# Performance work log

Measured on AMD Instinct MI355X. Metric: run time of the kernel, lower is better.

The kernel has to match this reference:

```python
import jax, jax.numpy as jnp
import numpy as np


def setup_inputs() -> dict:
    B, S, DK, DV, H = 2, 2048, 1024, 1024, 16
    ks = jax.random.split(jax.random.key(0), 7)
    keys = jax.random.normal(ks[0], (B, S, DK), jnp.float32)
    queries = jax.random.normal(ks[1], (B, S, DK), jnp.float32)
    values = jax.random.normal(ks[2], (B, S, DV), jnp.float32)
    # per-head projection weights, stored as [H, in, out] (torch Linear uses W.T; math-equivalent)
    WQ = jax.random.normal(ks[3], (H, DK, DK // H), jnp.float32) / np.sqrt(DK).astype(np.float32)
    WK = jax.random.normal(ks[4], (H, DK, DK // H), jnp.float32) / np.sqrt(DK).astype(np.float32)
    WV = jax.random.normal(ks[5], (H, DV, DV // H), jnp.float32) / np.sqrt(DV).astype(np.float32)
    WO = jax.random.normal(ks[6], (DV, DV), jnp.float32) / np.sqrt(DV).astype(np.float32)
    return {"keys": keys, "queries": queries, "values": values,
            "WQ": WQ, "WK": WK, "WV": WV, "WO": WO, "masking": 1}


def reference(keys, queries, values, WQ, WK, WV, WO, masking):
    B, Sq, _ = queries.shape
    Sk = keys.shape[1]
    # batched per-head projections (original loops over heads in Python)
    Q = jnp.einsum('bqd,hde->bhqe', queries, WQ)   # [B,H,Sq,dh]
    K = jnp.einsum('bkd,hde->bhke', keys, WK)      # [B,H,Sk,dh]
    V = jnp.einsum('bkd,hde->bhke', values, WV)    # [B,H,Sk,dvh]
    q_idx = jnp.arange(Sq)[:, None]
    k_idx = jnp.arange(Sk)[None, :]
    causal = k_idx <= q_idx
    # NOTE: original never applies the slope m; bias = (i - j) for i<=j else 0, same for all heads
    bias = jnp.where(causal, (k_idx - q_idx).astype(jnp.float32), 0.0)
    scale = np.float32(1.0 / np.sqrt(Sk))  # original divides by sqrt(keys.shape[1])
    y = (jnp.einsum('bhqe,bhke->bhqk', Q, K) + bias) * scale
    if masking:
        y = jnp.where(causal, y, -jnp.inf)
    # original: F.softmax(y, 1) on [B,Sq,Sk] -> softmax over the QUERY axis
    z = jax.nn.softmax(y, axis=2)
    out = jnp.einsum('bhqk,bhke->bhqe', z, V)      # [B,H,Sq,dvh]
    out = out.transpose(0, 2, 1, 3).reshape(B, Sq, -1)  # concat heads on last dim
    return out @ WO
```

## Files before the change

### kernel.cpp

```cpp
#include <hip/hip_runtime.h>
#include <math.h>

#define SEQ    2048
#define DMODEL 1024
#define NH     16
#define DH     64
#define NB     2
#define BHN    (NB*NH)

static constexpr float SCALE = 0.02209708691207961f;

typedef __attribute__((ext_vector_type(8))) short short8;
typedef __attribute__((ext_vector_type(4))) short short4v;
typedef __attribute__((ext_vector_type(4))) float f32x4;

__device__ __forceinline__ short f2bf(float f) {
    union { float f; unsigned u; } v; v.f = f;
    unsigned r = (v.u + 0x7FFFu + ((v.u >> 16) & 1u)) >> 16;
    return (short)r;
}

__device__ __forceinline__ unsigned pack_bf2(float a, float b) {
    union { float f; unsigned u; } ua, ub; ua.f = a; ub.f = b;
    return __builtin_amdgcn_perm(ub.u + 0x8000u, ua.u + 0x8000u, 0x07060302u);
}

__device__ __forceinline__ float bf2f(short s) {
    union { unsigned u; float f; } v; v.u = ((unsigned)(unsigned short)s) << 16;
    return v.f;
}

__device__ __forceinline__ void load16_lds(const short* g, short* l) {
    __builtin_amdgcn_global_load_lds(
        (const __attribute__((address_space(1))) unsigned int*)g,
        (__attribute__((address_space(3))) unsigned int*)l,
        16, 0, 0);
}

__device__ __forceinline__ void stage_rows(const short* g, short* s, int t, int ldg, int nIter) {
    int wave = t >> 6, lane = t & 63;
    #pragma unroll
    for (int i = 0; i < 4; ++i) {
        if (i >= nIter) break;
        int E   = i * 2048 + wave * 512 + lane * 8;
        int row = E >> 6;
        int blk = (lane & 7) ^ (row & 7);
        load16_lds(g + (size_t)row * ldg + blk * 8, s + i * 2048 + wave * 512);
    }
}

__device__ __forceinline__ short8 frag_sw(const short* s, int rowbase, int ks, int lane) {
    int m   = rowbase + (lane & 15);
    int q   = lane >> 4;
    int blk = (ks * 4 + q) ^ (m & 7);
    return *(const short8*)(s + m * 64 + blk * 8);
}

__device__ __forceinline__ void swizzle_tile(int x, int y, int& tile, int& bh) {
    int r = y >> 3;
    bh = (y & 7) * 4 + r;
    int xs = (r & 2) ? ((x + 16) & 31) : x;
    tile = (r & 1) ? (31 - xs) : xs;
}

__global__ __launch_bounds__(256) void convert_x(
    const float* __restrict__ q, const float* __restrict__ k, const float* __restrict__ v,
    short* __restrict__ Xq, short* __restrict__ Xk, short* __restrict__ Xv)
{
    const int z = blockIdx.z;
    const float* src = (z == 0) ? q : (z == 1) ? k : v;
    short* dst = (z == 0) ? Xq : (z == 1) ? Xk : Xv;
    size_t idx = ((size_t)blockIdx.x * 256 + threadIdx.x) * 8;
    float4 a = *(const float4*)(src + idx);
    float4 b = *(const float4*)(src + idx + 4);
    short8 o;
    o[0] = f2bf(a.x); o[1] = f2bf(a.y); o[2] = f2bf(a.z); o[3] = f2bf(a.w);
    o[4] = f2bf(b.x); o[5] = f2bf(b.y); o[6] = f2bf(b.z); o[7] = f2bf(b.w);
    *(short8*)(dst + idx) = o;
}

__global__ __launch_bounds__(256) void convert_w(
    const float* __restrict__ WQ, const float* __restrict__ WK,
    const float* __restrict__ WV, const float* __restrict__ WO,
    short* __restrict__ WQt, short* __restrict__ WKt,
    short* __restrict__ WVt, short* __restrict__ WOt)
{
    const int z = blockIdx.z;
    const int k0 = blockIdx.x * 64;
    const int ny = blockIdx.y;
    const float* W = (z == 0) ? WQ : (z == 1) ? WK : (z == 2) ? WV : WO;
    short* Wt = (z == 0) ? WQt : (z == 1) ? WKt : (z == 2) ? WVt : WOt;

    __shared__ float Ts[64][68];
    const int t = threadIdx.x;
    const int tr = t >> 4, tc4 = (t & 15) * 4;

    #pragma unroll
    for (int i = 0; i < 4; ++i) {
        int row = tr + i * 16;
        float4 v;
        if (z < 3) v = *(const float4*)(W + (size_t)ny * DMODEL * DH + (size_t)(k0 + row) * DH + tc4);
        else       v = *(const float4*)(W + (size_t)(k0 + row) * DMODEL + ny * 64 + tc4);
        Ts[tc4 + 0][row] = v.x; Ts[tc4 + 1][row] = v.y;
        Ts[tc4 + 2][row] = v.z; Ts[tc4 + 3][row] = v.w;
    }
    __syncthreads();
    #pragma unroll
    for (int i = 0; i < 4; ++i) {
        int nl = tr + i * 16;
        short4v o;
        o[0] = f2bf(Ts[nl][tc4 + 0]); o[1] = f2bf(Ts[nl][tc4 + 1]);
        o[2] = f2bf(Ts[nl][tc4 + 2]); o[3] = f2bf(Ts[nl][tc4 + 3]);
        *(short4v*)(Wt + (size_t)(ny * 64 + nl) * DMODEL + k0 + tc4) = o;
    }
}

__global__ __launch_bounds__(256) void gemm_nt(
    const short* __restrict__ A0, const short* __restrict__ A1, const short* __restrict__ A2,
    const short* __restrict__ B0, const short* __restrict__ B1, const short* __restrict__ B2,
    short* __restrict__ Y0, short* __restrict__ Y1, short* __restrict__ Y2,
    float* __restrict__ outF, int phase)
{
    const int z = blockIdx.z;
    const short* X  = (phase == 1) ? A0 : (z == 0) ? A0 : (z == 1) ? A1 : A2;
    const short* Wt = (phase == 1) ? B0 : (z == 0) ? B0 : (z == 1) ? B1 : B2;
    short* Y        = (z == 0) ? Y0 : (z == 1) ? Y1 : Y2;
    const bool vOrient = (phase == 0) && (z == 2);

    const int n0 = blockIdx.x * 128;
    const int m0 = blockIdx.y * 128;

    __shared__ short As[128 * 64];
    __shared__ short Bs[128 * 64];

    const int t = threadIdx.x;
    const int wave = t >> 6, lane = t & 63;
    const int wrow = (wave >> 1) * 64, wcol = (wave & 1) * 64;
    const int quad = lane >> 4, l15 = lane & 15;

    f32x4 acc[4][4];
    #pragma unroll
    for (int i = 0; i < 4; ++i)
        #pragma unroll
        for (int j = 0; j < 4; ++j)
            acc[i][j] = (f32x4)0.f;

    for (int k0 = 0; k0 < DMODEL; k0 += 64) {
        __syncthreads();
        stage_rows(X  + (size_t)m0 * DMODEL + k0, As, t, DMODEL, 4);
        stage_rows(Wt + (size_t)n0 * DMODEL + k0, Bs, t, DMODEL, 4);
        __syncthreads();
        if (!vOrient) {
            #pragma unroll
            for (int ks = 0; ks < 2; ++ks) {
                short8 xf[4], wf[4];
                #pragma unroll
                for (int i = 0; i < 4; ++i) xf[i] = frag_sw(As, wrow + i * 16, ks, lane);
                #pragma unroll
                for (int i = 0; i < 4; ++i) wf[i] = frag_sw(Bs, wcol + i * 16, ks, lane);
                #pragma unroll
                for (int a = 0; a < 4; ++a)
                    #pragma unroll
                    for (int b = 0; b < 4; ++b)
                        acc[a][b] = __builtin_amdgcn_mfma_f32_16x16x32_bf16(
                            wf[a], xf[b], acc[a][b], 0, 0, 0);
            }
        } else {
            #pragma unroll
            for (int ks = 0; ks < 2; ++ks) {
                short8 xf[4], wf[4];
                #pragma unroll
                for (int i = 0; i < 4; ++i) xf[i] = frag_sw(As, wrow + i * 16, ks, lane);
                #pragma unroll
                for (int i = 0; i < 4; ++i) wf[i] = frag_sw(Bs, wcol + i * 16, ks, lane);
                #pragma unroll
                for (int a = 0; a < 4; ++a)
                    #pragma unroll
                    for (int b = 0; b < 4; ++b)
                        acc[a][b] = __builtin_amdgcn_mfma_f32_16x16x32_bf16(
                            xf[a], wf[b], acc[a][b], 0, 0, 0);
            }
        }
    }

    if (vOrient) {
        #pragma unroll
        for (int a = 0; a < 4; ++a) {
            #pragma unroll
            for (int b = 0; b < 4; ++b) {
                int m = m0 + wrow + a * 16 + quad * 4;
                int n = n0 + wcol + b * 16 + l15;
                int bb = m >> 11, s = m & 2047, h = n >> 6, e = n & 63;
                short4v o;
                #pragma unroll
                for (int i = 0; i < 4; ++i) o[i] = f2bf(acc[a][b][i]);
                *(short4v*)(Y + ((size_t)((bb * NH + h) * DH + e)) * SEQ + s) = o;
            }
        }
    } else if (phase == 1) {
        #pragma unroll
        for (int a = 0; a < 4; ++a) {
            #pragma unroll
            for (int b = 0; b < 4; ++b) {
                int n = n0 + wcol + a * 16 + quad * 4;
                int m = m0 + wrow + b * 16 + l15;
                float4 o = make_float4(acc[a][b][0], acc[a][b][1], acc[a][b][2], acc[a][b][3]);
                *(float4*)(outF + (size_t)m * DMODEL + n) = o;
            }
        }
    } else {
        #pragma unroll
        for (int a = 0; a < 4; ++a) {
            #pragma unroll
            for (int b = 0; b < 4; ++b) {
                int n = n0 + wcol + a * 16 + quad * 4;
                int m = m0 + wrow + b * 16 + l15;
                int bb = m >> 11, s = m & 2047, h = n >> 6, e = n & 63;
                short4v o;
                #pragma unroll
                for (int i = 0; i < 4; ++i) o[i] = f2bf(acc[a][b][i]);
                *(short4v*)(Y + ((size_t)((bb * NH + h) * SEQ + s)) * DH + e) = o;
            }
        }
    }
}

template<int MODE>
__device__ __forceinline__ void stats_tile_w(
    const short* Qbuf, const short8 Kf[2], const float bias[4][4],
    float dsum[4], int lane, int wave16)
{
    const int quad = lane >> 4, l15 = lane & 15;
    f32x4 acc[4];
    #pragma unroll
    for (int nt = 0; nt < 4; ++nt) acc[nt] = (f32x4)0.f;
    #pragma unroll
    for (int ks = 0; ks < 2; ++ks) {
        #pragma unroll
        for (int nt = 0; nt < 4; ++nt)
            acc[nt] = __builtin_amdgcn_mfma_f32_16x16x32_bf16(
                Kf[ks], frag_sw(Qbuf, nt * 16, ks, lane), acc[nt], 0, 0, 0);
    }
    #pragma unroll
    for (int nt = 0; nt < 4; ++nt) {
        #pragma unroll
        for (int i = 0; i < 4; ++i) {
            float bi = bias[nt][i];
            float v = (MODE == 2) ? fmaf(acc[nt][i], SCALE, fminf(bi, 0.f))
                                  : fmaf(acc[nt][i], SCALE, bi);
            float e = __expf(v);
            if (MODE == 1)
                e = ((wave16 + quad * 4 + i) <= (nt * 16 + l15)) ? e : 0.f;
            dsum[i] += e;
        }
    }
}

__global__ __launch_bounds__(256) void stats_mfma(
    const short* __restrict__ Qg, const short* __restrict__ Kg,
    float* __restrict__ rDg, const int* __restrict__ mask_p)
{
    int kt, bh;
    swizzle_tile(blockIdx.x, blockIdx.y, kt, bh);
    const int k0 = kt * 64;
    const int masking = mask_p[0];

    __shared__ short Ks[64 * 64];
    __shared__ short Qs[2][64 * 64];

    const int t = threadIdx.x;
    const int wave = t >> 6, lane = t & 63;
    const int quad = lane >> 4, l15 = lane & 15;

    const int q0s = masking ? k0 : 0;
    stage_rows(Kg + ((size_t)bh * SEQ + k0) * DH, Ks, t, DH, 2);
    stage_rows(Qg + ((size_t)bh * SEQ + q0s) * DH, Qs[0], t, DH, 2);
    __syncthreads();

    short8 Kf[2];
    Kf[0] = frag_sw(Ks, wave * 16, 0, lane);
    Kf[1] = frag_sw(Ks, wave * 16, 1, lane);

    float bias[4][4];
    #pragma unroll
    for (int nt = 0; nt < 4; ++nt)
        #pragma unroll
        for (int i = 0; i < 4; ++i)
            bias[nt][i] = SCALE * (float)((k0 + wave * 16 + quad * 4 + i)
                                        - (q0s + nt * 16 + l15));

    float dsum[4] = {0.f, 0.f, 0.f, 0.f};
    const int nIter = (SEQ - q0s) / 64;
    for (int it = 0; it < nIter; ++it) {
        const int cur = it & 1;
        if (it > 0) __syncthreads();
        if (it + 1 < nIter)
            stage_rows(Qg + ((size_t)bh * SEQ + q0s + (it + 1) * 64) * DH, Qs[1 - cur], t, DH, 2);
        if (!masking)      stats_tile_w<2>(Qs[cur], Kf, bias, dsum, lane, wave * 16);
        else if (it == 0)  stats_tile_w<1>(Qs[cur], Kf, bias, dsum, lane, wave * 16);
        else               stats_tile_w<0>(Qs[cur], Kf, bias, dsum, lane, wave * 16);
        #pragma unroll
        for (int nt = 0; nt < 4; ++nt)
            #pragma unroll
            for (int i = 0; i < 4; ++i)
                bias[nt][i] -= 64.f * SCALE;
    }

    #pragma unroll
    for (int i = 0; i < 4; ++i) {
        float d = dsum[i];
        #pragma unroll
        for (int mm = 1; mm < 16; mm <<= 1) d += __shfl_xor(d, mm);
        dsum[i] = d;
    }
    if (l15 == 0) {
        const int kc = k0 + wave * 16 + quad * 4;
        float4 o = make_float4(1.f / dsum[0], 1.f / dsum[1], 1.f / dsum[2], 1.f / dsum[3]);
        *(float4*)(rDg + (size_t)bh * SEQ + kc) = o;
    }
}

__global__ __launch_bounds__(256) void scale_vt(
    short* __restrict__ Vt, const float* __restrict__ rDg)
{
    size_t base = ((size_t)blockIdx.x * 256 + threadIdx.x) * 8;
    int s = (int)(base & (SEQ - 1));
    int bh = (int)(base >> 17);
    short8 v = *(short8*)(Vt + base);
    const float* rp = rDg + (size_t)bh * SEQ + s;
    float4 r0 = *(const float4*)rp;
    float4 r1 = *(const float4*)(rp + 4);
    float rr[8] = {r0.x, r0.y, r0.z, r0.w, r1.x, r1.y, r1.z, r1.w};
    union { unsigned u[4]; short8 s8; } o;
    #pragma unroll
    for (int j = 0; j < 4; ++j)
        o.u[j] = pack_bf2(bf2f(v[2 * j]) * rr[2 * j], bf2f(v[2 * j + 1]) * rr[2 * j + 1]);
    *(short8*)(Vt + base) = o.s8;
}

template<int MODE>
__device__ __forceinline__ void attn_tile(
    const short* Kbuf, const short* Vbuf, short* Pw,
    const short8 Qf[2], const float bias[4][4], f32x4 oacc[4],
    int lane, int quad, int l15, int qloc)
{
    f32x4 sacc[4];
    #pragma unroll
    for (int mt = 0; mt < 4; ++mt) sacc[mt] = (f32x4)0.f;
    #pragma unroll
    for (int ks = 0; ks < 2; ++ks) {
        #pragma unroll
        for (int mt = 0; mt < 4; ++mt)
            sacc[mt] = __builtin_amdgcn_mfma_f32_16x16x32_bf16(
                frag_sw(Kbuf, mt * 16, ks, lane), Qf[ks], sacc[mt], 0, 0, 0);
    }
    __asm__ volatile("" ::: "memory");
    #pragma unroll
    for (int mt = 0; mt < 4; ++mt) {
        float p[4];
        #pragma unroll
        for (int i = 0; i < 4; ++i) {
            float bi = bias[mt][i];
            float v = (MODE == 2) ? fmaf(sacc[mt][i], SCALE, fminf(bi, 0.f))
                                  : fmaf(sacc[mt][i], SCALE, bi);
            float e = __expf(v);
            if (MODE == 1)
                e = ((mt * 16 + quad * 4 + i) <= qloc) ? e : 0.f;
            p[i] = e;
        }
        int blk = (2 * mt + (quad >> 1)) ^ (l15 & 7);
        *(uint2*)(Pw + l15 * 64 + blk * 8 + (quad & 1) * 4) =
            make_uint2(pack_bf2(p[0], p[1]), pack_bf2(p[2], p[3]));
    }
    __asm__ volatile("" ::: "memory");
    #pragma unroll
    for (int ks = 0; ks < 2; ++ks) {
        short8 pf = *(const short8*)(Pw + l15 * 64 + (((ks * 4 + quad) ^ (l15 & 7)) * 8));
        #pragma unroll
        for (int mt = 0; mt < 4; ++mt)
            oacc[mt] = __builtin_amdgcn_mfma_f32_16x16x32_bf16(
                frag_sw(Vbuf, mt * 16, ks, lane), pf, oacc[mt], 0, 0, 0);
    }
}

__global__ __launch_bounds__(256) void attn_mfma(
    const short* __restrict__ Qg, const short* __restrict__ Kg, const short* __restrict__ Vt,
    short* __restrict__ attnb, const int* __restrict__ mask_p)
{
    int qt, bh;
    swizzle_tile(blockIdx.x, blockIdx.y, qt, bh);
    const int b = bh / NH, h = bh % NH;
    const int q0 = qt * 64;
    const int masking = mask_p[0];

    __shared__ short Qs[64 * 64];
    __shared__ short Ks[2][64 * 64];
    __shared__ short Vts[2][64 * 64];

    const int t = threadIdx.x;
    const int wave = t >> 6, lane = t & 63;
    const int quad = lane >> 4, l15 = lane & 15;
    short* Pw = Qs + wave * 1024;
    const int qloc = wave * 16 + l15;

    stage_rows(Qg + ((size_t)bh * SEQ + q0) * DH, Qs, t, DH, 2);
    stage_rows(Kg + (size_t)bh * SEQ * DH, Ks[0], t, DH, 2);
    stage_rows(Vt + (size_t)bh * DH * SEQ, Vts[0], t, SEQ, 2);
    __syncthreads();

    short8 Qf[2];
    Qf[0] = frag_sw(Qs, wave * 16, 0, lane);
    Qf[1] = frag_sw(Qs, wave * 16, 1, lane);

    float bias[4][4];
    #pragma unroll
    for (int mt = 0; mt < 4; ++mt)
        #pragma unroll
        for (int i = 0; i < 4; ++i)
            bias[mt][i] = SCALE * (float)((mt * 16 + quad * 4 + i)
                                        - (q0 + qloc));

    f32x4 oacc[4];
    #pragma unroll
    for (int mt = 0; mt < 4; ++mt) oacc[mt] = (f32x4)0.f;

    const int nIter = masking ? (qt + 1) : (SEQ / 64);
    for (int it = 0; it < nIter; ++it) {
        const int cur = it & 1;
        if (it > 0) __syncthreads();
        if (it + 1 < nIter) {
            const int k0n = (it + 1) * 64;
            stage_rows(Kg + ((size_t)bh * SEQ + k0n) * DH, Ks[1 - cur], t, DH, 2);
            stage_rows(Vt + (size_t)bh * DH * SEQ + k0n, Vts[1 - cur], t, SEQ, 2);
        }
        if (!masking)       attn_tile<2>(Ks[cur], Vts[cur], Pw, Qf, bias, oacc, lane, quad, l15, qloc);
        else if (it == qt)  attn_tile<1>(Ks[cur], Vts[cur], Pw, Qf, bias, oacc, lane, quad, l15, qloc);
        else                attn_tile<0>(Ks[cur], Vts[cur], Pw, Qf, bias, oacc, lane, quad, l15, qloc);
        #pragma unroll
        for (int mt = 0; mt < 4; ++mt)
            #pragma unroll
            for (int i = 0; i < 4; ++i)
                bias[mt][i] += 64.f * SCALE;
    }

    #pragma unroll
    for (int mt = 0; mt < 4; ++mt) {
        int e = mt * 16 + quad * 4;
        int q = q0 + wave * 16 + l15;
        short4v o;
        #pragma unroll
        for (int i = 0; i < 4; ++i) o[i] = f2bf(oacc[mt][i]);
        *(short4v*)(attnb + ((size_t)(b * SEQ + q)) * DMODEL + h * DH + e) = o;
    }
}

extern "C" void kernel_launch(void* const* d_in, const int* in_sizes, int n_in,
                              void* d_out, int out_size, void* d_ws, size_t ws_size,
                              hipStream_t stream) {
    const float* keys    = (const float*)d_in[0];
    const float* queries = (const float*)d_in[1];
    const float* values  = (const float*)d_in[2];
    const float* WQ      = (const float*)d_in[3];
    const float* WK      = (const float*)d_in[4];
    const float* WV      = (const float*)d_in[5];
    const float* WO      = (const float*)d_in[6];
    const int*   mask_p  = (const int*)d_in[7];
    float* out = (float*)d_out;

    const size_t nX = (size_t)NB * SEQ * DMODEL;
    const size_t nW = (size_t)DMODEL * DMODEL;
    const size_t nQ = (size_t)BHN * SEQ * DH;

    short* ws = (short*)d_ws;
    short* Xq    = ws;
    short* Xk    = Xq + nX;
    short* Xv    = Xk + nX;
    short* WQt   = Xv + nX;
    short* WKt   = WQt + nW;
    short* WVt   = WKt + nW;
    short* WOt   = WVt + nW;
    short* Qg    = WOt + nW;
    short* Kg    = Qg + nQ;
    short* Vtg   = Kg + nQ;
    short* attnb = Vtg + nQ;
    float* rDg   = (float*)(attnb + nX);

    convert_x<<<dim3(2048, 1, 3), dim3(256), 0, stream>>>(queries, keys, values, Xq, Xk, Xv);
    convert_w<<<dim3(16, 16, 4), dim3(256), 0, stream>>>(WQ, WK, WV, WO, WQt, WKt, WVt, WOt);
    gemm_nt<<<dim3(8, 32, 3), dim3(256), 0, stream>>>(
        Xq, Xk, Xv, WQt, WKt, WVt, Qg, Kg, Vtg, nullptr, 0);
    stats_mfma<<<dim3(32, 32), dim3(256), 0, stream>>>(Qg, Kg, rDg, mask_p);
    scale_vt<<<dim3(2048), dim3(256), 0, stream>>>(Vtg, rDg);
    attn_mfma<<<dim3(32, 32), dim3(256), 0, stream>>>(Qg, Kg, Vtg, attnb, mask_p);
    gemm_nt<<<dim3(8, 32, 1), dim3(256), 0, stream>>>(
        attnb, nullptr, nullptr, WOt, nullptr, nullptr, nullptr, nullptr, nullptr, out, 1);
}
```

Baseline: 268.7 us.

## Fuse V scaling into stats kernel, use exp2, drop attention double buffering

The stats kernel now keeps the per-key reciprocal softmax denominators in shared memory and scales its own 64-column slice of Vt in place. This removes the separate scale_vt launch and the rD global buffer. Both softmax exponentials switch to exp2f, with log2(e) folded into the scale and bias constants. The attention kernel drops K/V double buffering in favour of a single buffer with two barriers per iteration, which cuts LDS use and may raise occupancy but loses overlap of loads with compute.

```diff
diff --git a/kernel.cpp b/kernel.cpp
--- a/kernel.cpp
+++ b/kernel.cpp
@@ -8,7 +8,8 @@
 #define NB     2
 #define BHN    (NB*NH)
 
-static constexpr float SCALE = 0.02209708691207961f;
+static constexpr float SCALE  = 0.02209708691207961f;
+static constexpr float SCALE2 = 0.02209708691207961f * 1.4426950408889634f;
 
 typedef __attribute__((ext_vector_type(8))) short short8;
 typedef __attribute__((ext_vector_type(4))) short short4v;
@@ -246,9 +247,9 @@
         #pragma unroll
         for (int i = 0; i < 4; ++i) {
             float bi = bias[nt][i];
-            float v = (MODE == 2) ? fmaf(acc[nt][i], SCALE, fminf(bi, 0.f))
-                                  : fmaf(acc[nt][i], SCALE, bi);
-            float e = __expf(v);
+            float v = (MODE == 2) ? fmaf(acc[nt][i], SCALE2, fminf(bi, 0.f))
+                                  : fmaf(acc[nt][i], SCALE2, bi);
+            float e = exp2f(v);
             if (MODE == 1)
                 e = ((wave16 + quad * 4 + i) <= (nt * 16 + l15)) ? e : 0.f;
             dsum[i] += e;
@@ -258,7 +259,7 @@
 
 __global__ __launch_bounds__(256) void stats_mfma(
     const short* __restrict__ Qg, const short* __restrict__ Kg,
-    float* __restrict__ rDg, const int* __restrict__ mask_p)
+    short* __restrict__ Vt, const int* __restrict__ mask_p)
 {
     int kt, bh;
     swizzle_tile(blockIdx.x, blockIdx.y, kt, bh);
@@ -267,6 +268,7 @@
 
     __shared__ short Ks[64 * 64];
     __shared__ short Qs[2][64 * 64];
+    __shared__ float rDs[64];
 
     const int t = threadIdx.x;
     const int wave = t >> 6, lane = t & 63;
@@ -286,8 +288,8 @@
     for (int nt = 0; nt < 4; ++nt)
         #pragma unroll
         for (int i = 0; i < 4; ++i)
-            bias[nt][i] = SCALE * (float)((k0 + wave * 16 + quad * 4 + i)
-                                        - (q0s + nt * 16 + l15));
+            bias[nt][i] = SCALE2 * (float)((k0 + wave * 16 + quad * 4 + i)
+                                         - (q0s + nt * 16 + l15));
 
     float dsum[4] = {0.f, 0.f, 0.f, 0.f};
     const int nIter = (SEQ - q0s) / 64;
@@ -303,7 +305,7 @@
         for (int nt = 0; nt < 4; ++nt)
             #pragma unroll
             for (int i = 0; i < 4; ++i)
-                bias[nt][i] -= 64.f * SCALE;
+                bias[nt][i] -= 64.f * SCALE2;
     }
 
     #pragma unroll
@@ -314,28 +316,25 @@
         dsum[i] = d;
     }
     if (l15 == 0) {
-        const int kc = k0 + wave * 16 + quad * 4;
+        const int kloc = wave * 16 + quad * 4;
         float4 o = make_float4(1.f / dsum[0], 1.f / dsum[1], 1.f / dsum[2], 1.f / dsum[3]);
-        *(float4*)(rDg + (size_t)bh * SEQ + kc) = o;
-    }
-}
-
-__global__ __launch_bounds__(256) void scale_vt(
-    short* __restrict__ Vt, const float* __restrict__ rDg)
-{
-    size_t base = ((size_t)blockIdx.x * 256 + threadIdx.x) * 8;
-    int s = (int)(base & (SEQ - 1));
-    int bh = (int)(base >> 17);
-    short8 v = *(short8*)(Vt + base);
-    const float* rp = rDg + (size_t)bh * SEQ + s;
-    float4 r0 = *(const float4*)rp;
-    float4 r1 = *(const float4*)(rp + 4);
-    float rr[8] = {r0.x, r0.y, r0.z, r0.w, r1.x, r1.y, r1.z, r1.w};
-    union { unsigned u[4]; short8 s8; } o;
-    #pragma unroll
-    for (int j = 0; j < 4; ++j)
-        o.u[j] = pack_bf2(bf2f(v[2 * j]) * rr[2 * j], bf2f(v[2 * j + 1]) * rr[2 * j + 1]);
-    *(short8*)(Vt + base) = o.s8;
+        *(float4*)&rDs[kloc] = o;
+    }
+    __syncthreads();
+
+    short* vp = Vt + (size_t)bh * DH * SEQ + k0;
+    #pragma unroll
+    for (int c = t; c < 512; c += 256) {
+        int e = c >> 3, sc = (c & 7) * 8;
+        short* p = vp + (size_t)e * SEQ + sc;
+        short8 v = *(short8*)p;
+        union { unsigned u[4]; short8 s8; } o;
+        #pragma unroll
+        for (int j = 0; j < 4; ++j)
+            o.u[j] = pack_bf2(bf2f(v[2 * j]) * rDs[sc + 2 * j],
+                              bf2f(v[2 * j + 1]) * rDs[sc + 2 * j + 1]);
+        *(short8*)p = o.s8;
+    }
 }
 
 template<int MODE>
@@ -361,9 +360,9 @@
         #pragma unroll
         for (int i = 0; i < 4; ++i) {
             float bi = bias[mt][i];
-            float v = (MODE == 2) ? fmaf(sacc[mt][i], SCALE, fminf(bi, 0.f))
-                                  : fmaf(sacc[mt][i], SCALE, bi);
-            float e = __expf(v);
+            float v = (MODE == 2) ? fmaf(sacc[mt][i], SCALE2, fminf(bi, 0.f))
+                                  : fmaf(sacc[mt][i], SCALE2, bi);
+            float e = exp2f(v);
             if (MODE == 1)
                 e = ((mt * 16 + quad * 4 + i) <= qloc) ? e : 0.f;
             p[i] = e;
@@ -394,8 +393,8 @@
     const int masking = mask_p[0];
 
     __shared__ short Qs[64 * 64];
-    __shared__ short Ks[2][64 * 64];
-    __shared__ short Vts[2][64 * 64];
+    __shared__ short Ks[64 * 64];
+    __shared__ short Vts[64 * 64];
 
     const int t = threadIdx.x;
     const int wave = t >> 6, lane = t & 63;
@@ -404,8 +403,6 @@
     const int qloc = wave * 16 + l15;
 
     stage_rows(Qg + ((size_t)bh * SEQ + q0) * DH, Qs, t, DH, 2);
-    stage_rows(Kg + (size_t)bh * SEQ * DH, Ks[0], t, DH, 2);
-    stage_rows(Vt + (size_t)bh * DH * SEQ, Vts[0], t, SEQ, 2);
     __syncthreads();
 
     short8 Qf[2];
@@ -417,8 +414,8 @@
     for (int mt = 0; mt < 4; ++mt)
         #pragma unroll
         for (int i = 0; i < 4; ++i)
-            bias[mt][i] = SCALE * (float)((mt * 16 + quad * 4 + i)
-                                        - (q0 + qloc));
+            bias[mt][i] = SCALE2 * (float)((mt * 16 + quad * 4 + i)
+                                         - (q0 + qloc));
 
     f32x4 oacc[4];
     #pragma unroll
@@ -426,21 +423,18 @@
 
     const int nIter = masking ? (qt + 1) : (SEQ / 64);
     for (int it = 0; it < nIter; ++it) {
-        const int cur = it & 1;
-        if (it > 0) __syncthreads();
-        if (it + 1 < nIter) {
-            const int k0n = (it + 1) * 64;
-            stage_rows(Kg + ((size_t)bh * SEQ + k0n) * DH, Ks[1 - cur], t, DH, 2);
-            stage_rows(Vt + (size_t)bh * DH * SEQ + k0n, Vts[1 - cur], t, SEQ, 2);
-        }
-        if (!masking)       attn_tile<2>(Ks[cur], Vts[cur], Pw, Qf, bias, oacc, lane, quad, l15, qloc);
-        else if (it == qt)  attn_tile<1>(Ks[cur], Vts[cur], Pw, Qf, bias, oacc, lane, quad, l15, qloc);
-        else                attn_tile<0>(Ks[cur], Vts[cur], Pw, Qf, bias, oacc, lane, quad, l15, qloc);
+        __syncthreads();
+        stage_rows(Kg + ((size_t)bh * SEQ + it * 64) * DH, Ks, t, DH, 2);
+        stage_rows(Vt + (size_t)bh * DH * SEQ + it * 64, Vts, t, SEQ, 2);
+        __syncthreads();
+        if (!masking)       attn_tile<2>(Ks, Vts, Pw, Qf, bias, oacc, lane, quad, l15, qloc);
+        else if (it == qt)  attn_tile<1>(Ks, Vts, Pw, Qf, bias, oacc, lane, quad, l15, qloc);
+        else                attn_tile<0>(Ks, Vts, Pw, Qf, bias, oacc, lane, quad, l15, qloc);
         #pragma unroll
         for (int mt = 0; mt < 4; ++mt)
             #pragma unroll
             for (int i = 0; i < 4; ++i)
-                bias[mt][i] += 64.f * SCALE;
+                bias[mt][i] += 64.f * SCALE2;
     }
 
     #pragma unroll
@@ -483,14 +477,12 @@
     short* Kg    = Qg + nQ;
     short* Vtg   = Kg + nQ;
     short* attnb = Vtg + nQ;
-    float* rDg   = (float*)(attnb + nX);
 
     convert_x<<<dim3(2048, 1, 3), dim3(256), 0, stream>>>(queries, keys, values, Xq, Xk, Xv);
     convert_w<<<dim3(16, 16, 4), dim3(256), 0, stream>>>(WQ, WK, WV, WO, WQt, WKt, WVt, WOt);
     gemm_nt<<<dim3(8, 32, 3), dim3(256), 0, stream>>>(
         Xq, Xk, Xv, WQt, WKt, WVt, Qg, Kg, Vtg, nullptr, 0);
-    stats_mfma<<<dim3(32, 32), dim3(256), 0, stream>>>(Qg, Kg, rDg, mask_p);
-    scale_vt<<<dim3(2048), dim3(256), 0, stream>>>(Vtg, rDg);
+    stats_mfma<<<dim3(32, 32), dim3(256), 0, stream>>>(Qg, Kg, Vtg, mask_p);
     attn_mfma<<<dim3(32, 32), dim3(256), 0, stream>>>(Qg, Kg, Vtg, attnb, mask_p);
     gemm_nt<<<dim3(8, 32, 1), dim3(256), 0, stream>>>(
         attnb, nullptr, nullptr, WOt, nullptr, nullptr, nullptr, nullptr, nullptr, out, 1);
```

Result: slower. 275.5 us (+2.5%).
